# Performance work log

Hardware: AMD Instinct MI355X
Metric: run time of the kernel (lower is better)

The kernel has to match this reference:

```python
import jax, jax.numpy as jnp
import numpy as np

B, C, Co, T, V, S, R, G = 64, 128, 128, 256, 25, 3, 16, 32
EPS = 1e-5


def setup_inputs() -> dict:
    key = jax.random.key(0)
    ks = jax.random.split(key, 12)
    sc = lambda fan: (2.0 / fan) ** 0.5  # kaiming fan_out-ish scale
    x = jax.random.normal(ks[0], (B, C, T, V), dtype=jnp.float32)
    Wq = jax.random.normal(ks[1], (S, R, C), dtype=jnp.float32) * sc(R)
    bq = jnp.zeros((S, R), dtype=jnp.float32)
    Wk = jax.random.normal(ks[2], (S, R, C), dtype=jnp.float32) * sc(R)
    bk = jnp.zeros((S, R), dtype=jnp.float32)
    Wv = jax.random.normal(ks[3], (S, Co, C), dtype=jnp.float32) * sc(Co)
    bv = jnp.zeros((S, Co), dtype=jnp.float32)
    Wr = jax.random.normal(ks[4], (S, Co, R), dtype=jnp.float32) * sc(Co)
    br = jnp.zeros((S, Co), dtype=jnp.float32)
    A = (jax.random.uniform(ks[5], (S, V, V), dtype=jnp.float32) < 0.15).astype(jnp.float32)
    alpha = jnp.zeros((1,), dtype=jnp.float32) + 0.1  # nonzero so relation path matters
    gn_w = jnp.full((Co,), 1e-6, dtype=jnp.float32)
    gn_b = jnp.zeros((Co,), dtype=jnp.float32)
    return {"x": x, "Wq": Wq, "bq": bq, "Wk": Wk, "bk": bk, "Wv": Wv, "bv": bv,
            "Wr": Wr, "br": br, "A": A, "alpha": alpha, "gn_w": gn_w, "gn_b": gn_b}


def reference(x, Wq, bq, Wk, bk, Wv, bv, Wr, br, A, alpha, gn_w, gn_b):
    # x: [B,C,T,V]. Mean over T commutes with the 1x1 conv (linear+bias).
    xm = x.mean(axis=2)                                          # [B,C,V]
    q = jnp.einsum('bcv,src->bsrv', xm, Wq) + bq[None, :, :, None]
    k = jnp.einsum('bcv,src->bsrv', xm, Wk) + bk[None, :, :, None]
    v = jnp.einsum('bctv,soc->bsotv', x, Wv) + bv[None, :, :, None, None]  # [B,S,Co,T,V]
    rel = jnp.tanh(q[..., :, None] - k[..., None, :])            # [B,S,R,V,V]
    relc = jnp.einsum('bsruv,sor->bsouv', rel, Wr) + br[None, :, :, None, None]
    relc = relc * alpha[0] + A[None, :, None, :, :]              # [B,S,Co,V,V]
    out = jnp.einsum('bsouv,bsotv->botu', relc, v)               # sum over subsets fused
    # GroupNorm(G, Co)
    o = out.reshape(B, G, Co // G, T, V)
    mu = o.mean(axis=(2, 3, 4), keepdims=True)
    var = ((o - mu) ** 2).mean(axis=(2, 3, 4), keepdims=True)
    o = ((o - mu) * jax.lax.rsqrt(var + EPS)).reshape(B, Co, T, V)
    o = o * gn_w[None, :, None, None] + gn_b[None, :, None, None]
    return jax.nn.relu(o + x)  # in==out -> identity residual
```

## Files before the change

kernel.cpp:

```cpp
#include <hip/hip_runtime.h>

#define BB 64
#define CC 128
#define CO 128
#define TTOT 256
#define VV 25
#define SS 3
#define RR 16
#define GG 32
#define EPSV 1e-5f

typedef __attribute__((ext_vector_type(8))) __bf16 bf16x8;
typedef __attribute__((ext_vector_type(4))) float f32x4;

static __device__ __forceinline__ ushort f2bf(float f) {
    unsigned u = __float_as_uint(f);
    u = (u + 0x7FFF + ((u >> 16) & 1)) >> 16;
    return (ushort)u;
}
static __device__ __forceinline__ ushort f2bf_fast(float f) {
    return (ushort)((__float_as_uint(f) + 0x8000u) >> 16);
}
static __device__ __forceinline__ float bf2f(ushort h) {
    return __uint_as_float(((unsigned)h) << 16);
}
static __device__ __forceinline__ f32x4 mfma16(bf16x8 a, bf16x8 b, f32x4 c) {
    return __builtin_amdgcn_mfma_f32_16x16x32_bf16(a, b, c, 0, 0, 0);
}
static __device__ __forceinline__ void bar_lds() {
    asm volatile("s_waitcnt lgkmcnt(0)" ::: "memory");
    __builtin_amdgcn_s_barrier();
}

__global__ __launch_bounds__(512) void k_xpose(const float* __restrict__ x,
                                               ushort* __restrict__ xg,
                                               float* __restrict__ xm) {
    int bid = blockIdx.x;
    int b = bid >> 4, c8 = bid & 15;
    int tid = threadIdx.x;
    __shared__ float sx[8 * 800];
    float xsum = 0.f;
    const float* xb = x + ((size_t)b * CC + c8 * 8) * (TTOT * VV);
    ushort* xo = xg + (size_t)bid * 8192 * 8;
    int cc = tid / VV, vv = tid % VV;
    for (int ti = 0; ti < 8; ++ti) {
        for (int i = tid; i < 1600; i += 512) {
            int c = i / 200, q = i % 200;
            *(float4*)&sx[c * 800 + q * 4] =
                *(const float4*)&xb[(size_t)c * (TTOT * VV) + ti * 800 + q * 4];
        }
        __syncthreads();
        for (int i = tid; i < 1024; i += 512) {
            int t = i >> 5, k = i & 31;
            union { ushort us[8]; int4 v4; } u;
            if (k < VV) {
#pragma unroll
                for (int c = 0; c < 8; ++c) u.us[c] = f2bf(sx[c * 800 + t * VV + k]);
            } else u.v4 = int4{0, 0, 0, 0};
            *(int4*)&xo[(size_t)((ti * 32 + t) * 32 + k) * 8] = u.v4;
        }
        if (tid < 200) {
#pragma unroll
            for (int t = 0; t < 32; ++t) xsum += sx[cc * 800 + t * VV + vv];
        }
        __syncthreads();
    }
    if (tid < 200) xm[((size_t)b * CC + c8 * 8 + cc) * VV + vv] = xsum * (1.0f / TTOT);
}

__global__ __launch_bounds__(512) void k_pack_wv(const float* __restrict__ Wv,
                                                 ushort* __restrict__ wvp) {
    int t = blockIdx.x * 512 + threadIdx.x;
    int lane = t & 63;
    int ks = (t >> 6) & 3;
    int mt = (t >> 8) & 1;
    int ob = (t >> 9) & 3;
    int s  = t >> 11;
    int o  = ob * 32 + mt * 16 + (lane & 15);
    int c0 = (ks * 4 + (lane >> 4)) * 8;
    const float* src = Wv + ((size_t)s * CO + o) * CC + c0;
    float4 a = *(const float4*)src;
    float4 b = *(const float4*)(src + 4);
    union { ushort us[8]; int4 v; } u;
    u.us[0] = f2bf(a.x); u.us[1] = f2bf(a.y); u.us[2] = f2bf(a.z); u.us[3] = f2bf(a.w);
    u.us[4] = f2bf(b.x); u.us[5] = f2bf(b.y); u.us[6] = f2bf(b.z); u.us[7] = f2bf(b.w);
    *(int4*)&wvp[(size_t)t * 8] = u.v;
}

__global__ __launch_bounds__(512) void k_qk(const float* __restrict__ xm,
    const float* __restrict__ Wq, const float* __restrict__ bq,
    const float* __restrict__ Wk, const float* __restrict__ bk,
    float* __restrict__ qb, float* __restrict__ kbuf) {
    int bs = blockIdx.x;
    int b = bs / SS, s = bs % SS;
    int tid = threadIdx.x;
    __shared__ float sxm[CC * VV];
    for (int i = tid; i < CC * VV; i += 512) sxm[i] = xm[(size_t)b * CC * VV + i];
    __syncthreads();
    if (tid < RR * VV) {
        int r = tid / VV, u = tid % VV;
        const float* wq = Wq + ((size_t)s * RR + r) * CC;
        const float* wk = Wk + ((size_t)s * RR + r) * CC;
        float aq = bq[s * RR + r], ak = bk[s * RR + r];
        for (int c = 0; c < CC; ++c) { float xv = sxm[c * VV + u]; aq += wq[c] * xv; ak += wk[c] * xv; }
        qb[bs * 400 + tid] = aq;
        kbuf[bs * 400 + tid] = ak;
    }
}

__global__ __launch_bounds__(256) void k_relcpack(const float* __restrict__ qb,
    const float* __restrict__ kbuf, const float* __restrict__ Wr,
    const float* __restrict__ br, const float* __restrict__ A,
    const float* __restrict__ alpha, const float* __restrict__ bv,
    ushort* __restrict__ rp) {
    int blk = blockIdx.x;
    int oc = blk & 7, bs = blk >> 3;
    int s = bs % SS;
    int tid = threadIdx.x;
    __shared__ float sq[RR * VV], sk[RR * VV];
    __shared__ float srel[RR][VV * VV];
    __shared__ ushort spack[16 * 1024];
    for (int i = tid; i < RR * VV; i += 256) { sq[i] = qb[bs * 400 + i]; sk[i] = kbuf[bs * 400 + i]; }
    __syncthreads();
    for (int i = tid; i < RR * VV * VV; i += 256) {
        int r = i / (VV * VV), uv = i % (VV * VV);
        srel[r][uv] = tanhf(sq[r * VV + uv / VV] - sk[r * VV + uv % VV]);
    }
    __syncthreads();
    float al = alpha[0];
    for (int i = tid; i < 512; i += 256) {
        int ol = i >> 5, u = i & 31;
        int o = oc * 16 + ol;
        ushort* dst = &spack[ol * 1024 + (u >> 4) * 512 + (u & 15) * 8];
        if (u < VV) {
            float acc[VV];
            float base = br[s * CO + o];
#pragma unroll
            for (int k = 0; k < VV; ++k) acc[k] = base;
            const float* wr = Wr + ((size_t)s * CO + o) * RR;
#pragma unroll
            for (int r = 0; r < RR; ++r) {
                float w = wr[r];
                const float* sr = &srel[r][u * VV];
#pragma unroll
                for (int k = 0; k < VV; ++k) acc[k] += w * sr[k];
            }
            const float* Ab = A + (size_t)s * VV * VV + u * VV;
            float vals[VV]; float rsum = 0.f;
#pragma unroll
            for (int k = 0; k < VV; ++k) { vals[k] = acc[k] * al + Ab[k]; rsum += vals[k]; }
            float bvt = bv[s * CO + o] * rsum;
#pragma unroll
            for (int kb4 = 0; kb4 < 4; ++kb4) {
                union { ushort us[8]; int4 v; } pk;
#pragma unroll
                for (int j = 0; j < 8; ++j) {
                    int kk = kb4 * 8 + j;
                    pk.us[j] = (kk < VV) ? f2bf(vals[kk])
                             : (kk == VV) ? f2bf(bvt) : (ushort)0;
                }
                *(int4*)&dst[kb4 * 128] = pk.v;
            }
        } else {
#pragma unroll
            for (int kb4 = 0; kb4 < 4; ++kb4)
                *(int4*)&dst[kb4 * 128] = int4{0, 0, 0, 0};
        }
    }
    __syncthreads();
    int4* dstg = (int4*)(rp + ((size_t)bs * CO + oc * 16) * 1024);
    const int4* srcs = (const int4*)spack;
    for (int i = tid; i < 2048; i += 256) dstg[i] = srcs[i];
}

__global__ __launch_bounds__(1024, 4) void k_main(const ushort* __restrict__ xg,
    const ushort* __restrict__ wvp, const ushort* __restrict__ rp,
    ushort* __restrict__ outw, float* __restrict__ stats) {
    int bid = blockIdx.x;
    int b = (bid & 7) + 8 * (bid >> 7);
    int tch = (bid >> 3) & 15;
    int tid = threadIdx.x;
    int w = tid >> 6, lane = tid & 63, g4 = lane >> 4, l15 = lane & 15;

    __shared__ ushort s_v[2 * 32 * 16 * 32];

    int csw = ((l15 ^ w) & 7) << 2;
    int wbase = (l15 * 16 + w) * 32;
    int k0a = (g4 * 4) ^ csw;
    int k0b = (16 + g4 * 4) ^ csw;
    int ra[2][2];
#pragma unroll
    for (int oi = 0; oi < 2; ++oi) {
        int ol = w * 2 + oi;
        int cr = ((ol ^ l15) & 7) << 2;
        int hi = (g4 << 3) ^ (cr & 24);
        int lo0 = hi | (cr & 4);
        ra[oi][0] = (ol * 16 + l15) * 32 + lo0;
        ra[oi][1] = ra[oi][0] ^ 4;
    }

    bf16x8 xf0[4], xf1[4];
    {
        const ushort* xgb = xg + ((size_t)(b * 16) * 8192 + tch * 512 + w * 32 + l15) * 8;
#pragma unroll
        for (int ks = 0; ks < 4; ++ks) {
            xf0[ks] = *(const bf16x8*)&xgb[(size_t)(ks * 4 + g4) * 65536];
            xf1[ks] = *(const bf16x8*)&xgb[(size_t)(ks * 4 + g4) * 65536 + 128];
        }
    }

    const ushort* wvl = wvp + lane * 8;
    const ushort* rpt = rp + ((size_t)(b * SS) * CO + w * 2) * 1024 + g4 * 128 + l15 * 8;
    bf16x8 wvf0[4], wvf1[4];
#pragma unroll
    for (int ks = 0; ks < 4; ++ks) {
        wvf0[ks] = *(const bf16x8*)&wvl[ks * 512];
        wvf1[ks] = *(const bf16x8*)&wvl[2048 + ks * 512];
    }
    bf16x8 r00 = *(const bf16x8*)&rpt[0];
    bf16x8 r01 = *(const bf16x8*)&rpt[512];
    bf16x8 r10 = *(const bf16x8*)&rpt[1024];
    bf16x8 r11 = *(const bf16x8*)&rpt[1536];

    f32x4 a00 = {0,0,0,0}, a01 = {0,0,0,0}, a10 = {0,0,0,0}, a11 = {0,0,0,0};

    auto pack4 = [&](f32x4 d, bool patch) -> uint2 {
        union { ushort us[4]; uint2 v; } p;
        p.us[0] = f2bf_fast(d[0]);
        p.us[1] = patch ? (ushort)0x3F80 : f2bf_fast(d[1]);
        p.us[2] = f2bf_fast(d[2]);
        p.us[3] = f2bf_fast(d[3]);
        return p.v;
    };
    auto gemm1 = [&](ushort* wbuf) {
        f32x4 d00 = {0,0,0,0}, d01 = {0,0,0,0}, d10 = {0,0,0,0}, d11 = {0,0,0,0};
        __builtin_amdgcn_s_setprio(1);
#pragma unroll
        for (int ks = 0; ks < 4; ++ks) {
            d00 = mfma16(xf0[ks], wvf0[ks], d00);
            d01 = mfma16(xf0[ks], wvf1[ks], d01);
            d10 = mfma16(xf1[ks], wvf0[ks], d10);
            d11 = mfma16(xf1[ks], wvf1[ks], d11);
        }
        __builtin_amdgcn_s_setprio(0);
        bool pt = (g4 == 2);
        *(uint2*)&wbuf[wbase + k0a]        = pack4(d00, false);
        *(uint2*)&wbuf[wbase + 8192 + k0a] = pack4(d01, false);
        *(uint2*)&wbuf[wbase + k0b]        = pack4(d10, pt);
        *(uint2*)&wbuf[wbase + 8192 + k0b] = pack4(d11, pt);
    };

    gemm1(s_v);

    int ss = 0, ob = 0;
    for (int st = 0; st < 12; ++st) {
        bar_lds();
        int ss1 = (ss == 2) ? 0 : ss + 1;
        int ob1 = (ss == 2) ? ob + 1 : ob;
        bool more = (st < 11);

        if (more) {
            const ushort* wb = wvl + (ss1 * 4 + ob1) * 4096;
#pragma unroll
            for (int ks = 0; ks < 4; ++ks) {
                wvf0[ks] = *(const bf16x8*)&wb[ks * 512];
                wvf1[ks] = *(const bf16x8*)&wb[2048 + ks * 512];
            }
        }

        {
            const ushort* rbuf = s_v + (st & 1) * 16384;
            union { uint2 q[2]; bf16x8 v; } av;
            av.q[0] = *(const uint2*)&rbuf[ra[0][0]];
            av.q[1] = *(const uint2*)&rbuf[ra[0][1]];
            __builtin_amdgcn_s_setprio(1);
            a00 = mfma16(av.v, r00, a00);
            a01 = mfma16(av.v, r01, a01);
            __builtin_amdgcn_s_setprio(0);
            av.q[0] = *(const uint2*)&rbuf[ra[1][0]];
            av.q[1] = *(const uint2*)&rbuf[ra[1][1]];
            __builtin_amdgcn_s_setprio(1);
            a10 = mfma16(av.v, r10, a10);
            a11 = mfma16(av.v, r11, a11);
            __builtin_amdgcn_s_setprio(0);
        }

        if (more) {
            const ushort* rb = rpt + ((size_t)ss1 * CO + ob1 * 32) * 1024;
            r00 = *(const bf16x8*)&rb[0];
            r01 = *(const bf16x8*)&rb[512];
            r10 = *(const bf16x8*)&rb[1024];
            r11 = *(const bf16x8*)&rb[1536];
        }

        if (ss == 2) {
            float ps = 0.f, pq = 0.f;
#pragma unroll
            for (int oi = 0; oi < 2; ++oi) {
                int o = ob * 32 + w * 2 + oi;
                size_t obase = (((size_t)b * CO + o) * TTOT + tch * 16 + g4 * 4) * VV;
#pragma unroll
                for (int ut = 0; ut < 2; ++ut) {
                    f32x4 av = (oi == 0) ? (ut == 0 ? a00 : a01) : (ut == 0 ? a10 : a11);
#pragma unroll
                    for (int r = 0; r < 4; ++r) {
                        float val = av[r];
                        ps += val; pq += val * val;
                        if (ut == 0 || l15 < 9)
                            outw[obase + (size_t)r * VV + ut * 16 + l15] = f2bf_fast(val);
                    }
                }
            }
            a00 = f32x4{0,0,0,0}; a01 = f32x4{0,0,0,0};
            a10 = f32x4{0,0,0,0}; a11 = f32x4{0,0,0,0};
#pragma unroll
            for (int off = 32; off > 0; off >>= 1) {
                ps += __shfl_down(ps, off, 64);
                pq += __shfl_down(pq, off, 64);
            }
            if (lane == 0) {
                int g = ob * 8 + (w >> 1);
                atomicAdd(&stats[b * (GG * 2) + g * 2], ps);
                atomicAdd(&stats[b * (GG * 2) + g * 2 + 1], pq);
            }
        }

        if (more) gemm1(s_v + ((st + 1) & 1) * 16384);

        ss = ss1; ob = ob1;
    }
}

__global__ __launch_bounds__(256) void k_final(float* __restrict__ out,
    const ushort* __restrict__ outw, const float* __restrict__ x,
    const float* __restrict__ stats,
    const float* __restrict__ gw, const float* __restrict__ gb) {
    size_t i = ((size_t)blockIdx.x * 256 + threadIdx.x) * 4;
    int o = (int)((i / (TTOT * VV)) % CO);
    int b = (int)(i / ((size_t)CO * TTOT * VV));
    int gg = o >> 2;
    float s0 = stats[b * (GG * 2) + gg * 2];
    float s1 = stats[b * (GG * 2) + gg * 2 + 1];
    const float inv = 1.0f / (4 * TTOT * VV);
    float mu = s0 * inv;
    float var = s1 * inv - mu * mu;
    float rs = rsqrtf(var + EPSV) * gw[o];
    float sh = gb[o] - mu * rs;

    ushort4 rw = *(const ushort4*)(outw + i);
    float4 xr = *(const float4*)(x + i);
    float4 res;
    res.x = fmaxf(bf2f(rw.x) * rs + sh + xr.x, 0.f);
    res.y = fmaxf(bf2f(rw.y) * rs + sh + xr.y, 0.f);
    res.z = fmaxf(bf2f(rw.z) * rs + sh + xr.z, 0.f);
    res.w = fmaxf(bf2f(rw.w) * rs + sh + xr.w, 0.f);
    *(float4*)(out + i) = res;
}

extern "C" void kernel_launch(void* const* d_in, const int* in_sizes, int n_in,
                              void* d_out, int out_size, void* d_ws, size_t ws_size,
                              hipStream_t stream) {
    const float* x     = (const float*)d_in[0];
    const float* Wq    = (const float*)d_in[1];
    const float* bq    = (const float*)d_in[2];
    const float* Wk    = (const float*)d_in[3];
    const float* bk    = (const float*)d_in[4];
    const float* Wv    = (const float*)d_in[5];
    const float* bv    = (const float*)d_in[6];
    const float* Wr    = (const float*)d_in[7];
    const float* br    = (const float*)d_in[8];
    const float* A     = (const float*)d_in[9];
    const float* alpha = (const float*)d_in[10];
    const float* gw    = (const float*)d_in[11];
    const float* gb    = (const float*)d_in[12];
    float* out = (float*)d_out;

    float*  xm    = (float*)d_ws;
    float*  stats = xm + (size_t)BB * CC * VV;
    ushort* wvp   = (ushort*)(stats + (size_t)BB * GG * 2);
    ushort* rp    = wvp + 49152;
    ushort* outw  = rp + (size_t)BB * SS * CO * 1024;
    ushort* xg    = outw + (size_t)BB * CO * TTOT * VV;
    float*  qb    = (float*)outw;
    float*  kbuf  = qb + (size_t)BB * SS * RR * VV;

    hipMemsetAsync(stats, 0, (size_t)BB * GG * 2 * sizeof(float), stream);
    k_xpose<<<BB * 16, 512, 0, stream>>>(x, xg, xm);
    k_pack_wv<<<12, 512, 0, stream>>>(Wv, wvp);
    k_qk<<<BB * SS, 512, 0, stream>>>(xm, Wq, bq, Wk, bk, qb, kbuf);
    k_relcpack<<<BB * SS * 8, 256, 0, stream>>>(qb, kbuf, Wr, br, A, alpha, bv, rp);
    k_main<<<1024, 1024, 0, stream>>>(xg, wvp, rp, outw, stats);
    k_final<<<(BB * CO * TTOT * VV) / (256 * 4), 256, 0, stream>>>(out, outw, x, stats, gw, gb);
}
```

Measured before the change: 428.2 us.

## Split main kernel into smaller 512-thread blocks over half-size time chunks

Reworks k_main from 1024-thread blocks covering 16 time steps and 32 output channels per stage into 512-thread blocks covering 8 time steps and 16 channels, with twice the blocks and twice the pipeline stages. The LDS staging buffer is shrunk and re-laid out with a padded row stride of 528 to keep bank spreading. The aim is more, lighter blocks for better occupancy and scheduling. The cost is that the second MFMA now runs on 16-row tiles with only 8 valid time rows, so half of that work is discarded, and per-stage barrier and reload overhead doubles.

New measurement: 536.2 us. 25.2% more time.

```diff
diff --git a/kernel.cpp b/kernel.cpp
--- a/kernel.cpp
+++ b/kernel.cpp
@@ -173,35 +173,35 @@
     for (int i = tid; i < 2048; i += 256) dstg[i] = srcs[i];
 }
 
-__global__ __launch_bounds__(1024, 4) void k_main(const ushort* __restrict__ xg,
+__global__ __launch_bounds__(512, 4) void k_main(const ushort* __restrict__ xg,
     const ushort* __restrict__ wvp, const ushort* __restrict__ rp,
     ushort* __restrict__ outw, float* __restrict__ stats) {
     int bid = blockIdx.x;
-    int b = (bid & 7) + 8 * (bid >> 7);
-    int tch = (bid >> 3) & 15;
+    int b = (bid & 7) + 8 * (bid >> 8);
+    int tch = (bid >> 3) & 31;
     int tid = threadIdx.x;
     int w = tid >> 6, lane = tid & 63, g4 = lane >> 4, l15 = lane & 15;
 
-    __shared__ ushort s_v[2 * 32 * 16 * 32];
+    __shared__ ushort s_v[2 * 16 * 528];
 
     int csw = ((l15 ^ w) & 7) << 2;
-    int wbase = (l15 * 16 + w) * 32;
+    int wbase = l15 * 528 + w * 32;
     int k0a = (g4 * 4) ^ csw;
     int k0b = (16 + g4 * 4) ^ csw;
     int ra[2][2];
 #pragma unroll
     for (int oi = 0; oi < 2; ++oi) {
         int ol = w * 2 + oi;
-        int cr = ((ol ^ l15) & 7) << 2;
-        int hi = (g4 << 3) ^ (cr & 24);
-        int lo0 = hi | (cr & 4);
-        ra[oi][0] = (ol * 16 + l15) * 32 + lo0;
+        int tt = l15 & 7;
+        int cr = ((ol ^ tt) & 7) << 2;
+        int lo0 = ((g4 << 3) ^ (cr & 24)) | (cr & 4);
+        ra[oi][0] = ol * 528 + tt * 32 + lo0;
         ra[oi][1] = ra[oi][0] ^ 4;
     }
 
     bf16x8 xf0[4], xf1[4];
     {
-        const ushort* xgb = xg + ((size_t)(b * 16) * 8192 + tch * 512 + w * 32 + l15) * 8;
+        const ushort* xgb = xg + ((size_t)(b * 16) * 8192 + tch * 256 + w * 32 + l15) * 8;
 #pragma unroll
         for (int ks = 0; ks < 4; ++ks) {
             xf0[ks] = *(const bf16x8*)&xgb[(size_t)(ks * 4 + g4) * 65536];
@@ -211,12 +211,9 @@
 
     const ushort* wvl = wvp + lane * 8;
     const ushort* rpt = rp + ((size_t)(b * SS) * CO + w * 2) * 1024 + g4 * 128 + l15 * 8;
-    bf16x8 wvf0[4], wvf1[4];
-#pragma unroll
-    for (int ks = 0; ks < 4; ++ks) {
-        wvf0[ks] = *(const bf16x8*)&wvl[ks * 512];
-        wvf1[ks] = *(const bf16x8*)&wvl[2048 + ks * 512];
-    }
+    bf16x8 wvf[4];
+#pragma unroll
+    for (int ks = 0; ks < 4; ++ks) wvf[ks] = *(const bf16x8*)&wvl[ks * 512];
     bf16x8 r00 = *(const bf16x8*)&rpt[0];
     bf16x8 r01 = *(const bf16x8*)&rpt[512];
     bf16x8 r10 = *(const bf16x8*)&rpt[1024];
@@ -233,43 +230,36 @@
         return p.v;
     };
     auto gemm1 = [&](ushort* wbuf) {
-        f32x4 d00 = {0,0,0,0}, d01 = {0,0,0,0}, d10 = {0,0,0,0}, d11 = {0,0,0,0};
+        f32x4 d0 = {0,0,0,0}, d1 = {0,0,0,0};
         __builtin_amdgcn_s_setprio(1);
 #pragma unroll
         for (int ks = 0; ks < 4; ++ks) {
-            d00 = mfma16(xf0[ks], wvf0[ks], d00);
-            d01 = mfma16(xf0[ks], wvf1[ks], d01);
-            d10 = mfma16(xf1[ks], wvf0[ks], d10);
-            d11 = mfma16(xf1[ks], wvf1[ks], d11);
+            d0 = mfma16(xf0[ks], wvf[ks], d0);
+            d1 = mfma16(xf1[ks], wvf[ks], d1);
         }
         __builtin_amdgcn_s_setprio(0);
         bool pt = (g4 == 2);
-        *(uint2*)&wbuf[wbase + k0a]        = pack4(d00, false);
-        *(uint2*)&wbuf[wbase + 8192 + k0a] = pack4(d01, false);
-        *(uint2*)&wbuf[wbase + k0b]        = pack4(d10, pt);
-        *(uint2*)&wbuf[wbase + 8192 + k0b] = pack4(d11, pt);
+        *(uint2*)&wbuf[wbase + k0a] = pack4(d0, false);
+        *(uint2*)&wbuf[wbase + k0b] = pack4(d1, pt);
     };
 
     gemm1(s_v);
 
     int ss = 0, ob = 0;
-    for (int st = 0; st < 12; ++st) {
+    for (int st = 0; st < 24; ++st) {
         bar_lds();
         int ss1 = (ss == 2) ? 0 : ss + 1;
         int ob1 = (ss == 2) ? ob + 1 : ob;
-        bool more = (st < 11);
+        bool more = (st < 23);
 
         if (more) {
-            const ushort* wb = wvl + (ss1 * 4 + ob1) * 4096;
-#pragma unroll
-            for (int ks = 0; ks < 4; ++ks) {
-                wvf0[ks] = *(const bf16x8*)&wb[ks * 512];
-                wvf1[ks] = *(const bf16x8*)&wb[2048 + ks * 512];
-            }
+            const ushort* wb = wvl + (ss1 * 4 + (ob1 >> 1)) * 4096 + (ob1 & 1) * 2048;
+#pragma unroll
+            for (int ks = 0; ks < 4; ++ks) wvf[ks] = *(const bf16x8*)&wb[ks * 512];
         }
 
         {
-            const ushort* rbuf = s_v + (st & 1) * 16384;
+            const ushort* rbuf = s_v + (st & 1) * (16 * 528);
             union { uint2 q[2]; bf16x8 v; } av;
             av.q[0] = *(const uint2*)&rbuf[ra[0][0]];
             av.q[1] = *(const uint2*)&rbuf[ra[0][1]];
@@ -286,7 +276,7 @@
         }
 
         if (more) {
-            const ushort* rb = rpt + ((size_t)ss1 * CO + ob1 * 32) * 1024;
+            const ushort* rb = rpt + ((size_t)ss1 * CO + ob1 * 16) * 1024;
             r00 = *(const bf16x8*)&rb[0];
             r01 = *(const bf16x8*)&rb[512];
             r10 = *(const bf16x8*)&rb[1024];
@@ -297,35 +287,37 @@
             float ps = 0.f, pq = 0.f;
 #pragma unroll
             for (int oi = 0; oi < 2; ++oi) {
-                int o = ob * 32 + w * 2 + oi;
-                size_t obase = (((size_t)b * CO + o) * TTOT + tch * 16 + g4 * 4) * VV;
+                int o = ob * 16 + w * 2 + oi;
+                size_t obase = (((size_t)b * CO + o) * TTOT + tch * 8 + g4 * 4) * VV;
 #pragma unroll
                 for (int ut = 0; ut < 2; ++ut) {
                     f32x4 av = (oi == 0) ? (ut == 0 ? a00 : a01) : (ut == 0 ? a10 : a11);
-#pragma unroll
-                    for (int r = 0; r < 4; ++r) {
-                        float val = av[r];
-                        ps += val; pq += val * val;
-                        if (ut == 0 || l15 < 9)
-                            outw[obase + (size_t)r * VV + ut * 16 + l15] = f2bf_fast(val);
+                    if (g4 < 2) {
+#pragma unroll
+                        for (int r = 0; r < 4; ++r) {
+                            float val = av[r];
+                            ps += val; pq += val * val;
+                            if (ut == 0 || l15 < 9)
+                                outw[obase + (size_t)r * VV + ut * 16 + l15] = f2bf_fast(val);
+                        }
                     }
                 }
             }
             a00 = f32x4{0,0,0,0}; a01 = f32x4{0,0,0,0};
             a10 = f32x4{0,0,0,0}; a11 = f32x4{0,0,0,0};
 #pragma unroll
-            for (int off = 32; off > 0; off >>= 1) {
+            for (int off = 16; off > 0; off >>= 1) {
                 ps += __shfl_down(ps, off, 64);
                 pq += __shfl_down(pq, off, 64);
             }
             if (lane == 0) {
-                int g = ob * 8 + (w >> 1);
+                int g = ob * 4 + (w >> 1);
                 atomicAdd(&stats[b * (GG * 2) + g * 2], ps);
                 atomicAdd(&stats[b * (GG * 2) + g * 2 + 1], pq);
             }
         }
 
-        if (more) gemm1(s_v + ((st + 1) & 1) * 16384);
+        if (more) gemm1(s_v + ((st + 1) & 1) * (16 * 528));
 
         ss = ss1; ob = ob1;
     }
@@ -389,6 +381,6 @@
     k_pack_wv<<<12, 512, 0, stream>>>(Wv, wvp);
     k_qk<<<BB * SS, 512, 0, stream>>>(xm, Wq, bq, Wk, bk, qb, kbuf);
     k_relcpack<<<BB * SS * 8, 256, 0, stream>>>(qb, kbuf, Wr, br, A, alpha, bv, rp);
-    k_main<<<1024, 1024, 0, stream>>>(xg, wvp, rp, outw, stats);
+    k_main<<<2048, 512, 0, stream>>>(xg, wvp, rp, outw, stats);
     k_final<<<(BB * CO * TTOT * VV) / (256 * 4), 256, 0, stream>>>(out, outw, x, stats, gw, gb);
 }
```

## Drop bf16 transposed x copy; load fp32 x directly in main kernel

Applied to the files above, without the earlier changes.

Removes the k_xpose pass that wrote a bf16 channel-interleaved copy of x, replacing it with a lightweight per-(b,c) mean kernel. k_main now reads fp32 x directly with strided per-channel scalar loads and converts to bf16 in registers. The q/k projection is fused into k_relcpack (computed redundantly per o-chunk block), and the LDS staging of the packed relation matrix is replaced by direct global stores. This trades a full extra read+write of x for less coalesced 8-channel strided loads in the main kernel and redundant q/k computation.

Result: slower. 528.6 us (+23.5%).

```diff
diff --git a/kernel.cpp b/kernel.cpp
--- a/kernel.cpp
+++ b/kernel.cpp
@@ -32,40 +32,31 @@
     __builtin_amdgcn_s_barrier();
 }
 
-__global__ __launch_bounds__(512) void k_xpose(const float* __restrict__ x,
-                                               ushort* __restrict__ xg,
+__global__ __launch_bounds__(256) void k_xmean(const float* __restrict__ x,
                                                float* __restrict__ xm) {
-    int bid = blockIdx.x;
-    int b = bid >> 4, c8 = bid & 15;
-    int tid = threadIdx.x;
-    __shared__ float sx[8 * 800];
-    float xsum = 0.f;
-    const float* xb = x + ((size_t)b * CC + c8 * 8) * (TTOT * VV);
-    ushort* xo = xg + (size_t)bid * 8192 * 8;
-    int cc = tid / VV, vv = tid % VV;
-    for (int ti = 0; ti < 8; ++ti) {
-        for (int i = tid; i < 1600; i += 512) {
-            int c = i / 200, q = i % 200;
-            *(float4*)&sx[c * 800 + q * 4] =
-                *(const float4*)&xb[(size_t)c * (TTOT * VV) + ti * 800 + q * 4];
-        }
-        __syncthreads();
-        for (int i = tid; i < 1024; i += 512) {
-            int t = i >> 5, k = i & 31;
-            union { ushort us[8]; int4 v4; } u;
-            if (k < VV) {
-#pragma unroll
-                for (int c = 0; c < 8; ++c) u.us[c] = f2bf(sx[c * 800 + t * VV + k]);
-            } else u.v4 = int4{0, 0, 0, 0};
-            *(int4*)&xo[(size_t)((ti * 32 + t) * 32 + k) * 8] = u.v4;
-        }
-        if (tid < 200) {
-#pragma unroll
-            for (int t = 0; t < 32; ++t) xsum += sx[cc * 800 + t * VV + vv];
-        }
-        __syncthreads();
-    }
-    if (tid < 200) xm[((size_t)b * CC + c8 * 8 + cc) * VV + vv] = xsum * (1.0f / TTOT);
+    int bc = blockIdx.x;
+    const float* xp = x + (size_t)bc * (TTOT * VV);
+    int t = threadIdx.x;
+    float a[VV];
+    const float* row = xp + t * VV;
+#pragma unroll
+    for (int v = 0; v < VV; ++v) a[v] = row[v];
+#pragma unroll
+    for (int v = 0; v < VV; ++v) {
+#pragma unroll
+        for (int off = 32; off > 0; off >>= 1) a[v] += __shfl_down(a[v], off, 64);
+    }
+    __shared__ float sm[4][VV];
+    int wave = t >> 6, lane = t & 63;
+    if (lane == 0) {
+#pragma unroll
+        for (int v = 0; v < VV; ++v) sm[wave][v] = a[v];
+    }
+    __syncthreads();
+    if (t < VV) {
+        float s = sm[0][t] + sm[1][t] + sm[2][t] + sm[3][t];
+        xm[(size_t)bc * VV + t] = s * (1.0f / TTOT);
+    }
 }
 
 __global__ __launch_bounds__(512) void k_pack_wv(const float* __restrict__ Wv,
@@ -87,51 +78,48 @@
     *(int4*)&wvp[(size_t)t * 8] = u.v;
 }
 
-__global__ __launch_bounds__(512) void k_qk(const float* __restrict__ xm,
+__global__ __launch_bounds__(256) void k_relcpack(const float* __restrict__ xm,
     const float* __restrict__ Wq, const float* __restrict__ bq,
     const float* __restrict__ Wk, const float* __restrict__ bk,
-    float* __restrict__ qb, float* __restrict__ kbuf) {
-    int bs = blockIdx.x;
+    const float* __restrict__ Wr, const float* __restrict__ br,
+    const float* __restrict__ A, const float* __restrict__ alpha,
+    const float* __restrict__ bv, ushort* __restrict__ rp) {
+    int blk = blockIdx.x;
+    int oc = blk & 7, bs = blk >> 3;
     int b = bs / SS, s = bs % SS;
     int tid = threadIdx.x;
     __shared__ float sxm[CC * VV];
-    for (int i = tid; i < CC * VV; i += 512) sxm[i] = xm[(size_t)b * CC * VV + i];
-    __syncthreads();
-    if (tid < RR * VV) {
-        int r = tid / VV, u = tid % VV;
-        const float* wq = Wq + ((size_t)s * RR + r) * CC;
-        const float* wk = Wk + ((size_t)s * RR + r) * CC;
-        float aq = bq[s * RR + r], ak = bk[s * RR + r];
-        for (int c = 0; c < CC; ++c) { float xv = sxm[c * VV + u]; aq += wq[c] * xv; ak += wk[c] * xv; }
-        qb[bs * 400 + tid] = aq;
-        kbuf[bs * 400 + tid] = ak;
-    }
-}
-
-__global__ __launch_bounds__(256) void k_relcpack(const float* __restrict__ qb,
-    const float* __restrict__ kbuf, const float* __restrict__ Wr,
-    const float* __restrict__ br, const float* __restrict__ A,
-    const float* __restrict__ alpha, const float* __restrict__ bv,
-    ushort* __restrict__ rp) {
-    int blk = blockIdx.x;
-    int oc = blk & 7, bs = blk >> 3;
-    int s = bs % SS;
-    int tid = threadIdx.x;
     __shared__ float sq[RR * VV], sk[RR * VV];
     __shared__ float srel[RR][VV * VV];
-    __shared__ ushort spack[16 * 1024];
-    for (int i = tid; i < RR * VV; i += 256) { sq[i] = qb[bs * 400 + i]; sk[i] = kbuf[bs * 400 + i]; }
+
+    for (int i = tid; i < CC * VV; i += 256) sxm[i] = xm[(size_t)b * CC * VV + i];
     __syncthreads();
+
+    if (tid < 200) {
+#pragma unroll
+        for (int it = 0; it < 2; ++it) {
+            int idx = tid + it * 200;
+            int r = idx / VV, u = idx % VV;
+            const float* wq = Wq + ((size_t)s * RR + r) * CC;
+            const float* wk = Wk + ((size_t)s * RR + r) * CC;
+            float aq = bq[s * RR + r], ak = bk[s * RR + r];
+            for (int c = 0; c < CC; ++c) { float xv = sxm[c * VV + u]; aq += wq[c] * xv; ak += wk[c] * xv; }
+            sq[idx] = aq; sk[idx] = ak;
+        }
+    }
+    __syncthreads();
+
     for (int i = tid; i < RR * VV * VV; i += 256) {
         int r = i / (VV * VV), uv = i % (VV * VV);
         srel[r][uv] = tanhf(sq[r * VV + uv / VV] - sk[r * VV + uv % VV]);
     }
     __syncthreads();
+
     float al = alpha[0];
     for (int i = tid; i < 512; i += 256) {
         int ol = i >> 5, u = i & 31;
         int o = oc * 16 + ol;
-        ushort* dst = &spack[ol * 1024 + (u >> 4) * 512 + (u & 15) * 8];
+        ushort* dst = rp + ((size_t)bs * CO + o) * 1024 + (u >> 4) * 512 + (u & 15) * 8;
         if (u < VV) {
             float acc[VV];
             float base = br[s * CO + o];
@@ -167,13 +155,9 @@
                 *(int4*)&dst[kb4 * 128] = int4{0, 0, 0, 0};
         }
     }
-    __syncthreads();
-    int4* dstg = (int4*)(rp + ((size_t)bs * CO + oc * 16) * 1024);
-    const int4* srcs = (const int4*)spack;
-    for (int i = tid; i < 2048; i += 256) dstg[i] = srcs[i];
-}
-
-__global__ __launch_bounds__(1024, 4) void k_main(const ushort* __restrict__ xg,
+}
+
+__global__ __launch_bounds__(1024, 4) void k_main(const float* __restrict__ x,
     const ushort* __restrict__ wvp, const ushort* __restrict__ rp,
     ushort* __restrict__ outw, float* __restrict__ stats) {
     int bid = blockIdx.x;
@@ -201,11 +185,20 @@
 
     bf16x8 xf0[4], xf1[4];
     {
-        const ushort* xgb = xg + ((size_t)(b * 16) * 8192 + tch * 512 + w * 32 + l15) * 8;
+        const float* xb = x + (size_t)b * CC * (TTOT * VV) + (tch * 16 + w) * VV;
+        bool k1ok = (l15 < 9);
 #pragma unroll
         for (int ks = 0; ks < 4; ++ks) {
-            xf0[ks] = *(const bf16x8*)&xgb[(size_t)(ks * 4 + g4) * 65536];
-            xf1[ks] = *(const bf16x8*)&xgb[(size_t)(ks * 4 + g4) * 65536 + 128];
+            int c0 = (ks * 4 + g4) * 8;
+            union { ushort us[8]; bf16x8 v; } u0, u1;
+#pragma unroll
+            for (int cc = 0; cc < 8; ++cc) {
+                const float* p = xb + (size_t)(c0 + cc) * (TTOT * VV);
+                u0.us[cc] = f2bf(p[l15]);
+                u1.us[cc] = k1ok ? f2bf(p[16 + l15]) : (ushort)0;
+            }
+            xf0[ks] = u0.v;
+            xf1[ks] = u1.v;
         }
     }
 
@@ -380,15 +373,11 @@
     ushort* wvp   = (ushort*)(stats + (size_t)BB * GG * 2);
     ushort* rp    = wvp + 49152;
     ushort* outw  = rp + (size_t)BB * SS * CO * 1024;
-    ushort* xg    = outw + (size_t)BB * CO * TTOT * VV;
-    float*  qb    = (float*)outw;
-    float*  kbuf  = qb + (size_t)BB * SS * RR * VV;
 
     hipMemsetAsync(stats, 0, (size_t)BB * GG * 2 * sizeof(float), stream);
-    k_xpose<<<BB * 16, 512, 0, stream>>>(x, xg, xm);
+    k_xmean<<<BB * CC, 256, 0, stream>>>(x, xm);
     k_pack_wv<<<12, 512, 0, stream>>>(Wv, wvp);
-    k_qk<<<BB * SS, 512, 0, stream>>>(xm, Wq, bq, Wk, bk, qb, kbuf);
-    k_relcpack<<<BB * SS * 8, 256, 0, stream>>>(qb, kbuf, Wr, br, A, alpha, bv, rp);
-    k_main<<<1024, 1024, 0, stream>>>(xg, wvp, rp, outw, stats);
+    k_relcpack<<<BB * SS * 8, 256, 0, stream>>>(xm, Wq, bq, Wk, bk, Wr, br, A, alpha, bv, rp);
+    k_main<<<1024, 1024, 0, stream>>>(x, wvp, rp, outw, stats);
     k_final<<<(BB * CO * TTOT * VV) / (256 * 4), 256, 0, stream>>>(out, outw, x, stats, gw, gb);
 }
```
